# Kernel tuning notes

Measured on AMD Instinct MI355X. Metric: run time of the kernel, lower is better.

## Reference

```python
import jax, jax.numpy as jnp
import numpy as np

N_NODES = 100000
N_EDGES = 1600000
F_IN, HID, N_CLS = 128, 64, 40


def gcn_conv(x, src, dst, W, b, n_nodes):
    # x: [N, Fin] -> [N, Fout]; edges already include self-loops.
    h = x @ W  # [N, Fout]
    ones = jnp.ones_like(src, dtype=h.dtype)
    deg = jax.ops.segment_sum(ones, dst, num_segments=n_nodes)  # [N]
    dinv = jnp.where(deg > 0, jax.lax.rsqrt(deg), 0.0)
    norm = dinv[src] * dinv[dst]  # [E]
    msg = h[src] * norm[:, None]  # gather + scale
    out = jax.ops.segment_sum(msg, dst, num_segments=n_nodes)  # scatter-sum
    return out + b


def setup_inputs() -> dict:
    key = jax.random.key(0)
    ks = jax.random.split(key, 8)
    x = jax.random.normal(ks[0], (N_NODES, F_IN), dtype=jnp.float32)
    edge_index = jax.random.randint(ks[1], (2, N_EDGES), 0, N_NODES, dtype=jnp.int64)

    def glorot(k, fi, fo):
        s = float(np.sqrt(6.0 / (fi + fo)))
        return jax.random.uniform(k, (fi, fo), jnp.float32, -s, s)

    return {
        "x": x,
        "edge_index": edge_index,
        "W1": glorot(ks[2], F_IN, HID), "b1": jnp.zeros((HID,), jnp.float32),
        "W2": glorot(ks[3], HID, HID), "b2": jnp.zeros((HID,), jnp.float32),
        "W3": glorot(ks[4], HID, N_CLS), "b3": jnp.zeros((N_CLS,), jnp.float32),
    }


def reference(x, edge_index, W1, b1, W2, b2, W3, b3):
    n = x.shape[0]
    loop = jnp.arange(n, dtype=edge_index.dtype)
    src = jnp.concatenate([edge_index[0], loop])  # add self-loops
    dst = jnp.concatenate([edge_index[1], loop])
    # layer 1..3: GCNConv -> relu -> dropout(eval: identity)
    h = jax.nn.relu(gcn_conv(x, src, dst, W1, b1, n))
    h = jax.nn.relu(gcn_conv(h, src, dst, W2, b2, n))
    h = jax.nn.relu(gcn_conv(h, src, dst, W3, b3, n))
    return jax.nn.log_softmax(h, axis=1)
```

## Files before the change

kernel.cpp:

```cpp
#include <hip/hip_runtime.h>
#include <math.h>

typedef _Float16 half8   __attribute__((ext_vector_type(8)));
typedef float    float4v __attribute__((ext_vector_type(4)));

#define NPB   196
#define CAP   4096
#define DIVM  342393ull

static __device__ __forceinline__ unsigned short f32_to_f16u(float f) {
    _Float16 h = (_Float16)f;
    return __builtin_bit_cast(unsigned short, h);
}

static __device__ __forceinline__ int bkt_of(int d) {
    return (int)(((unsigned long long)(unsigned)d * DIVM) >> 26);
}


__global__ __launch_bounds__(256) void bin_edges(
    const int* __restrict__ src, const int* __restrict__ dst,
    int* __restrict__ bcur, unsigned int* __restrict__ bint, int E, int NB)
{
    __shared__ int h[512];
    __shared__ int rbase[512];
    const int tid = threadIdx.x;
    h[tid] = 0; h[tid + 256] = 0;
    __syncthreads();

    const int chunk = (E + (int)gridDim.x - 1) / (int)gridDim.x;
    const int base  = (int)blockIdx.x * chunk;
    int end = base + chunk; if (end > E) end = E;

    for (int i = base + tid; i < end; i += 256)
        atomicAdd(&h[bkt_of(dst[i])], 1);
    __syncthreads();

    for (int j = tid; j < NB; j += 256) {
        int c = h[j];
        rbase[j] = c ? atomicAdd(&bcur[j], c) : 0;
        h[j] = 0;
    }
    __syncthreads();

    for (int i = base + tid; i < end; i += 256) {
        int d = dst[i];
        int bkt = bkt_of(d);
        int low = d - bkt * NPB;
        int pos = rbase[bkt] + atomicAdd(&h[bkt], 1);
        if (pos < CAP)
            bint[(size_t)bkt * CAP + pos] =
                ((unsigned int)src[i] << 8) | (unsigned int)low;
    }
}


__global__ __launch_bounds__(256) void build_csr(
    const unsigned int* __restrict__ bint, const int* __restrict__ bcur,
    int2* __restrict__ rp2, float* __restrict__ dinv, int* __restrict__ es, int n)
{
    __shared__ int cnt[256];
    __shared__ int sc[256];
    __shared__ int cur[256];
    const int b = blockIdx.x, tid = threadIdx.x;
    int total = bcur[b]; if (total > CAP) total = CAP;
    const unsigned int* bp = bint + (size_t)b * CAP;
    int* ep = es + (size_t)b * CAP;
    const int base = b * CAP;

    cnt[tid] = 0;
    __syncthreads();
    for (int i = tid; i < total; i += 256)
        atomicAdd(&cnt[bp[i] & 255], 1);
    __syncthreads();

    int v = (tid < NPB) ? cnt[tid] : 0;
    sc[tid] = v;
    __syncthreads();
    for (int off = 1; off < 256; off <<= 1) {
        int x = (tid >= off) ? sc[tid - off] : 0;
        __syncthreads();
        sc[tid] += x;
        __syncthreads();
    }
    int excl = sc[tid] - v;
    int node = b * NPB + tid;
    if (tid < NPB && node < n) {
        rp2[node]  = make_int2(base + excl, base + excl + v);
        dinv[node] = rsqrtf((float)(v + 1));
    }
    cur[tid] = excl;
    __syncthreads();

    for (int i = tid; i < total; i += 256) {
        unsigned int p = bp[i];
        int pos = atomicAdd(&cur[p & 255], 1);
        ep[pos] = (int)(p >> 8);
    }
}


template<int KK, int NT, int STRIDE, int MOUT, bool INF32>
__global__ __launch_bounds__(256) void gemm_t(
    const void* __restrict__ Xin, const float* __restrict__ W,
    const float* __restrict__ dinv, unsigned short* __restrict__ H, int n)
{
    constexpr int KS = KK >> 5;
    __shared__ __align__(16) unsigned short ldsA[4 * KS * 512];
    const int tid = threadIdx.x;
    const int n0  = blockIdx.x * 64;
    const int wv   = tid >> 6;
    const int lane = tid & 63;
    const int q8 = (lane >> 4) << 3, mc = lane & 15;

    half8 bf[NT * KS];
    #pragma unroll
    for (int u = 0; u < NT; ++u)
        #pragma unroll
        for (int s = 0; s < KS; ++s) {
            const int col = (u << 4) + mc;
            #pragma unroll
            for (int j = 0; j < 8; ++j)
                bf[u * KS + s][j] = (col < MOUT)
                    ? (_Float16)W[((s << 5) + q8 + j) * MOUT + col] : (_Float16)0;
        }

    {
        const int rl = tid >> 3;
        const int kl = tid & 7;
        #pragma unroll
        for (int rb = 0; rb < 64; rb += 32) {
            int r = rl + rb;
            int node = n0 + r;
            int t = r >> 4, m = r & 15;
            if (INF32) {
                #pragma unroll
                for (int kq8 = 0; kq8 < (KK >> 2); kq8 += 8) {
                    int k0 = (kl + kq8) << 2;
                    unsigned short h[4] = {0, 0, 0, 0};
                    if (node < n) {
                        const float* xp = (const float*)Xin + (size_t)node * KK + k0;
                        float4v v = *(const float4v*)xp;
                        #pragma unroll
                        for (int i = 0; i < 4; ++i) h[i] = f32_to_f16u(v[i]);
                    }
                    int s = k0 >> 5, q = (k0 >> 3) & 3, j0 = k0 & 7;
                    int lds_lane = (q << 4) | m;
                    unsigned short* p = &ldsA[((t * KS + s) << 9) + (lds_lane << 3) + j0];
                    *(uint2*)p = make_uint2((unsigned)h[0] | ((unsigned)h[1] << 16),
                                            (unsigned)h[2] | ((unsigned)h[3] << 16));
                }
            } else {
                uint4 v = make_uint4(0, 0, 0, 0);
                if (node < n)
                    v = *(const uint4*)((const unsigned short*)Xin + (size_t)node * KK + (kl << 3));
                int k0 = kl << 3;
                int s = k0 >> 5, q = (k0 >> 3) & 3;
                unsigned short* p = &ldsA[((t * KS + s) << 9) + ((((q << 4) | m)) << 3)];
                *(uint4*)p = v;
            }
        }
    }

    __syncthreads();

    float4v acc[NT];
    #pragma unroll
    for (int u = 0; u < NT; ++u) acc[u] = (float4v){0.f, 0.f, 0.f, 0.f};

    #pragma unroll
    for (int s = 0; s < KS; ++s) {
        half8 a = *(const half8*)&ldsA[((wv * KS + s) << 9) + (lane << 3)];
        #pragma unroll
        for (int u = 0; u < NT; ++u)
            acc[u] = __builtin_amdgcn_mfma_f32_16x16x32_f16(a, bf[u * KS + s], acc[u], 0, 0, 0);
    }

    const int quad = lane >> 4;
    #pragma unroll
    for (int reg = 0; reg < 4; ++reg) {
        int node = n0 + (wv << 4) + (quad << 2) + reg;
        if (node >= n) continue;
        float dv = dinv[node];
        #pragma unroll
        for (int u = 0; u < NT; ++u) {
            int col = (u << 4) + mc;
            if (col < MOUT)
                H[(size_t)node * STRIDE + col] = f32_to_f16u(acc[u][reg] * dv);
        }
    }
}


template<int MOUT, int ROWU4>
__global__ __launch_bounds__(256) void gather_t(
    const int2* __restrict__ rp2, const int* __restrict__ es,
    const unsigned short* __restrict__ H, const float* __restrict__ dinv,
    const float* __restrict__ bias, unsigned short* __restrict__ Aout, int n)
{
    const int lane   = threadIdx.x & 63;
    const int half   = lane >> 5;
    const int lane32 = lane & 31;
    const int slot   = (lane >> 3) & 3;
    const int c8     = lane & 7;
    const bool act   = c8 < ROWU4;
    const uint4* H4  = (const uint4*)H;

    float bi[8];
    #pragma unroll
    for (int i = 0; i < 8; ++i) bi[i] = bias[(c8 << 3) + i];

    const half8 hz = {(_Float16)0, (_Float16)0, (_Float16)0, (_Float16)0,
                      (_Float16)0, (_Float16)0, (_Float16)0, (_Float16)0};

    const int TW2 = (int)(gridDim.x << 3);
    for (int nb = (((int)blockIdx.x << 2) + ((int)threadIdx.x >> 6)) << 1; nb < n; nb += TW2) {
        const int node = nb + half;
        const int2 e = rp2[node];
        const float dv = dinv[node];

        half8 hacc = hz;
        if (slot == 0 && act)
            hacc = __builtin_bit_cast(half8, H4[(size_t)node * ROWU4 + c8]);

        for (int cb = e.x; cb < e.y; cb += 32) {
            const int rem = e.y - cb;
            int eidx = cb + lane32; if (eidx > e.y - 1) eidx = e.y - 1;
            const int ei = es[eidx];
            #pragma unroll
            for (int j = 0; j < 8; ++j) {
                const int idx = (j << 2) + slot;
                const int s = __shfl(ei, (half << 5) + idx, 64);
                if (idx < rem && act)
                    hacc = hacc + __builtin_bit_cast(half8, H4[(size_t)s * ROWU4 + c8]);
            }
        }

        #pragma unroll
        for (int step = 8; step <= 16; step <<= 1) {
            uint4 u = __builtin_bit_cast(uint4, hacc);
            uint4 o;
            o.x = __shfl_xor(u.x, step, 64);
            o.y = __shfl_xor(u.y, step, 64);
            o.z = __shfl_xor(u.z, step, 64);
            o.w = __shfl_xor(u.w, step, 64);
            hacc = hacc + __builtin_bit_cast(half8, o);
        }

        if (slot == 0) {
            unsigned short o[8];
            #pragma unroll
            for (int i = 0; i < 8; ++i)
                o[i] = f32_to_f16u(fmaxf((float)hacc[i] * dv + bi[i], 0.0f));
            uint4 w;
            w.x = (unsigned int)o[0] | ((unsigned int)o[1] << 16);
            w.y = (unsigned int)o[2] | ((unsigned int)o[3] << 16);
            w.z = (unsigned int)o[4] | ((unsigned int)o[5] << 16);
            w.w = (unsigned int)o[6] | ((unsigned int)o[7] << 16);
            ((uint4*)Aout)[(size_t)node * 8 + c8] = w;
        }
    }
}


template<int MOUT, int ROWU4>
__global__ __launch_bounds__(256) void gather_softmax(
    const int2* __restrict__ rp2, const int* __restrict__ es,
    const unsigned short* __restrict__ H, const float* __restrict__ dinv,
    const float* __restrict__ bias, float* __restrict__ out, int n)
{
    const int lane   = threadIdx.x & 63;
    const int half   = lane >> 5;
    const int lane32 = lane & 31;
    const int slot   = (lane >> 3) & 3;
    const int c8     = lane & 7;
    const bool act   = c8 < ROWU4;
    const uint4* H4  = (const uint4*)H;

    float bi[8];
    #pragma unroll
    for (int i = 0; i < 8; ++i) {
        int col = (c8 << 3) + i;
        bi[i] = (col < MOUT) ? bias[col] : 0.0f;
    }

    const half8 hz = {(_Float16)0, (_Float16)0, (_Float16)0, (_Float16)0,
                      (_Float16)0, (_Float16)0, (_Float16)0, (_Float16)0};

    const int TW2 = (int)(gridDim.x << 3);
    for (int nb = (((int)blockIdx.x << 2) + ((int)threadIdx.x >> 6)) << 1; nb < n; nb += TW2) {
        const int node = nb + half;
        const int2 e = rp2[node];
        const float dv = dinv[node];

        half8 hacc = hz;
        if (slot == 0 && act)
            hacc = __builtin_bit_cast(half8, H4[(size_t)node * ROWU4 + c8]);

        for (int cb = e.x; cb < e.y; cb += 32) {
            const int rem = e.y - cb;
            int eidx = cb + lane32; if (eidx > e.y - 1) eidx = e.y - 1;
            const int ei = es[eidx];
            #pragma unroll
            for (int j = 0; j < 8; ++j) {
                const int idx = (j << 2) + slot;
                const int s = __shfl(ei, (half << 5) + idx, 64);
                if (idx < rem && act)
                    hacc = hacc + __builtin_bit_cast(half8, H4[(size_t)s * ROWU4 + c8]);
            }
        }

        #pragma unroll
        for (int step = 8; step <= 16; step <<= 1) {
            uint4 u = __builtin_bit_cast(uint4, hacc);
            uint4 o;
            o.x = __shfl_xor(u.x, step, 64);
            o.y = __shfl_xor(u.y, step, 64);
            o.z = __shfl_xor(u.z, step, 64);
            o.w = __shfl_xor(u.w, step, 64);
            hacc = hacc + __builtin_bit_cast(half8, o);
        }

        float z[8]; float m = -INFINITY;
        #pragma unroll
        for (int i = 0; i < 8; ++i) {
            int col = (c8 << 3) + i;
            z[i] = (col < MOUT && act) ? fmaxf((float)hacc[i] * dv + bi[i], 0.0f)
                                       : -INFINITY;
            m = fmaxf(m, z[i]);
        }
        m = fmaxf(m, __shfl_xor(m, 1, 64));
        m = fmaxf(m, __shfl_xor(m, 2, 64));
        m = fmaxf(m, __shfl_xor(m, 4, 64));
        float s = 0.0f;
        #pragma unroll
        for (int i = 0; i < 8; ++i) s += expf(z[i] - m);
        s += __shfl_xor(s, 1, 64);
        s += __shfl_xor(s, 2, 64);
        s += __shfl_xor(s, 4, 64);
        float ls = logf(s) + m;
        if (slot == 0 && c8 < (MOUT + 7) / 8) {
            float* op = out + (size_t)node * MOUT + (c8 << 3);
            float4v o0 = {z[0] - ls, z[1] - ls, z[2] - ls, z[3] - ls};
            float4v o1 = {z[4] - ls, z[5] - ls, z[6] - ls, z[7] - ls};
            *(float4v*)op = o0;
            *(float4v*)(op + 4) = o1;
        }
    }
}


extern "C" void kernel_launch(void* const* d_in, const int* in_sizes, int n_in,
                              void* d_out, int out_size, void* d_ws, size_t ws_size,
                              hipStream_t stream)
{
    const float* x  = (const float*)d_in[0];
    const int*   ei = (const int*)  d_in[1];
    const float* W1 = (const float*)d_in[2];
    const float* b1 = (const float*)d_in[3];
    const float* W2 = (const float*)d_in[4];
    const float* b2 = (const float*)d_in[5];
    const float* W3 = (const float*)d_in[6];
    const float* b3 = (const float*)d_in[7];

    const int F_IN = 128;
    const int n = in_sizes[0] / F_IN;
    const int E = in_sizes[1] / 2;
    const int* src = ei;
    const int* dst = ei + E;
    float* out = (float*)d_out;

    const int NB = (n + NPB - 1) / NPB;

    auto align = [](size_t v) { return (v + 255) & ~(size_t)255; };
    char* w = (char*)d_ws;
    size_t off = 0;
    float*          dinv = (float*)(w + off);          off = align(off + (size_t)n * 4);
    unsigned short* H1   = (unsigned short*)(w + off); off = align(off + (size_t)n * 64 * 2);
    unsigned short* A    = (unsigned short*)(w + off); off = align(off + (size_t)n * 64 * 2);
    unsigned short* H3   = (unsigned short*)(w + off); off = align(off + (size_t)n * 40 * 2);
    int2*           rp2  = (int2*)(w + off);           off = align(off + (size_t)n * 8);
    int*            es   = (int*)(w + off);            off = align(off + (size_t)NB * CAP * 4);
    unsigned int*   bint = (unsigned int*)(w + off);   off = align(off + (size_t)NB * CAP * 4);
    int*            bcur = (int*)(w + off);            off = align(off + (size_t)1024 * 4);
    unsigned short* H2   = H1;

    const int BLK = 256;
    auto cdiv = [](int a, int b) { return (a + b - 1) / b; };
    const int GB = cdiv(n, 64);
    const int GG = 2048;

    hipMemsetAsync(bcur, 0, (size_t)1024 * 4, stream);
    bin_edges<<<512, BLK, 0, stream>>>(src, dst, bcur, bint, E, NB);
    build_csr<<<NB, BLK, 0, stream>>>(bint, bcur, rp2, dinv, es, n);

    gemm_t<128, 4, 64, 64, true><<<GB, BLK, 0, stream>>>(x, W1, dinv, H1, n);
    gather_t<64, 8><<<GG, BLK, 0, stream>>>(rp2, es, H1, dinv, b1, A, n);

    gemm_t<64, 4, 64, 64, false><<<GB, BLK, 0, stream>>>(A, W2, dinv, H2, n);
    gather_t<64, 8><<<GG, BLK, 0, stream>>>(rp2, es, H2, dinv, b2, A, n);

    gemm_t<64, 3, 40, 40, false><<<GB, BLK, 0, stream>>>(A, W3, dinv, H3, n);
    gather_softmax<40, 5><<<GG, BLK, 0, stream>>>(rp2, es, H3, dinv, b3, out, n);
}
```

Baseline: 283.1 us.

## Stage edge binning and CSR build through LDS for coalesced global writes

Buckets change from 196 nodes per bucket (chosen with a magic-multiply divide) to 256 nodes per bucket using a shift. Each bin_edges block now takes a fixed 8192-edge chunk read with int4 loads. It sorts payloads locally in LDS by bucket using a prefix scan, then writes them out linearly so the global scatter lands in contiguous runs. build_csr likewise stages the bucket's edges in LDS and writes the sorted source list back contiguously. This is meant to cut the cost of uncoalesced scattered global writes, in exchange for more LDS per block (lower occupancy) and a larger bucket capacity.

```diff
diff --git a/kernel.cpp b/kernel.cpp
--- a/kernel.cpp
+++ b/kernel.cpp
@@ -4,53 +4,88 @@
 typedef _Float16 half8   __attribute__((ext_vector_type(8)));
 typedef float    float4v __attribute__((ext_vector_type(4)));
 
-#define NPB   196
-#define CAP   4096
-#define DIVM  342393ull
+#define CAP   6144
+#define EPB   8192
 
 static __device__ __forceinline__ unsigned short f32_to_f16u(float f) {
     _Float16 h = (_Float16)f;
     return __builtin_bit_cast(unsigned short, h);
 }
 
-static __device__ __forceinline__ int bkt_of(int d) {
-    return (int)(((unsigned long long)(unsigned)d * DIVM) >> 26);
-}
-
 
 __global__ __launch_bounds__(256) void bin_edges(
     const int* __restrict__ src, const int* __restrict__ dst,
     int* __restrict__ bcur, unsigned int* __restrict__ bint, int E, int NB)
 {
+    __shared__ unsigned int pay[EPB];
+    __shared__ unsigned int targ[EPB];
     __shared__ int h[512];
+    __shared__ int h2[512];
+    __shared__ int sc[512];
     __shared__ int rbase[512];
-    const int tid = threadIdx.x;
+
+    const int tid  = threadIdx.x;
+    const int base = (int)blockIdx.x * EPB;
+    int end = base + EPB; if (end > E) end = E;
+    const int total = end - base;
+    const int L4 = total & ~3;
+
     h[tid] = 0; h[tid + 256] = 0;
-    __syncthreads();
-
-    const int chunk = (E + (int)gridDim.x - 1) / (int)gridDim.x;
-    const int base  = (int)blockIdx.x * chunk;
-    int end = base + chunk; if (end > E) end = E;
-
-    for (int i = base + tid; i < end; i += 256)
-        atomicAdd(&h[bkt_of(dst[i])], 1);
-    __syncthreads();
+    h2[tid] = 0; h2[tid + 256] = 0;
+    __syncthreads();
+
+    for (int i = tid << 2; i < L4; i += 1024) {
+        int4 d4 = *(const int4*)(dst + base + i);
+        atomicAdd(&h[d4.x >> 8], 1);
+        atomicAdd(&h[d4.y >> 8], 1);
+        atomicAdd(&h[d4.z >> 8], 1);
+        atomicAdd(&h[d4.w >> 8], 1);
+    }
+    for (int i = L4 + tid; i < total; i += 256)
+        atomicAdd(&h[dst[base + i] >> 8], 1);
+    __syncthreads();
+
+    int v0 = h[tid], v1 = h[tid + 256];
+    sc[tid] = v0; sc[tid + 256] = v1;
+    __syncthreads();
+    for (int off = 1; off < 512; off <<= 1) {
+        int x0 = (tid >= off) ? sc[tid - off] : 0;
+        int x1 = (tid + 256 >= off) ? sc[tid + 256 - off] : 0;
+        __syncthreads();
+        sc[tid] += x0; sc[tid + 256] += x1;
+        __syncthreads();
+    }
 
     for (int j = tid; j < NB; j += 256) {
         int c = h[j];
         rbase[j] = c ? atomicAdd(&bcur[j], c) : 0;
-        h[j] = 0;
-    }
-    __syncthreads();
-
-    for (int i = base + tid; i < end; i += 256) {
-        int d = dst[i];
-        int bkt = bkt_of(d);
-        int low = d - bkt * NPB;
-        int pos = rbase[bkt] + atomicAdd(&h[bkt], 1);
-        if (pos < CAP)
-            bint[(size_t)bkt * CAP + pos] =
-                ((unsigned int)src[i] << 8) | (unsigned int)low;
+    }
+    __syncthreads();
+
+    {
+        auto place = [&](int d, int s) {
+            int bkt  = d >> 8;
+            int rank = atomicAdd(&h2[bkt], 1);
+            int loc  = sc[bkt] - h[bkt] + rank;
+            pay[loc] = ((unsigned int)s << 8) | (unsigned int)(d & 255);
+            unsigned int t = (unsigned int)(rbase[bkt] + rank);
+            targ[loc] = (t < (unsigned int)CAP)
+                      ? (unsigned int)bkt * CAP + t : 0xFFFFFFFFu;
+        };
+        for (int i = tid << 2; i < L4; i += 1024) {
+            int4 d4 = *(const int4*)(dst + base + i);
+            int4 s4 = *(const int4*)(src + base + i);
+            place(d4.x, s4.x); place(d4.y, s4.y);
+            place(d4.z, s4.z); place(d4.w, s4.w);
+        }
+        for (int i = L4 + tid; i < total; i += 256)
+            place(dst[base + i], src[base + i]);
+    }
+    __syncthreads();
+
+    for (int i = tid; i < total; i += 256) {
+        unsigned int t = targ[i];
+        if (t != 0xFFFFFFFFu) bint[t] = pay[i];
     }
 }
 
@@ -62,6 +97,8 @@
     __shared__ int cnt[256];
     __shared__ int sc[256];
     __shared__ int cur[256];
+    __shared__ unsigned int pin[CAP];
+    __shared__ int pout[CAP];
     const int b = blockIdx.x, tid = threadIdx.x;
     int total = bcur[b]; if (total > CAP) total = CAP;
     const unsigned int* bp = bint + (size_t)b * CAP;
@@ -70,11 +107,14 @@
 
     cnt[tid] = 0;
     __syncthreads();
-    for (int i = tid; i < total; i += 256)
-        atomicAdd(&cnt[bp[i] & 255], 1);
-    __syncthreads();
-
-    int v = (tid < NPB) ? cnt[tid] : 0;
+    for (int i = tid; i < total; i += 256) {
+        unsigned int v = bp[i];
+        pin[i] = v;
+        atomicAdd(&cnt[v & 255], 1);
+    }
+    __syncthreads();
+
+    int v = cnt[tid];
     sc[tid] = v;
     __syncthreads();
     for (int off = 1; off < 256; off <<= 1) {
@@ -84,8 +124,8 @@
         __syncthreads();
     }
     int excl = sc[tid] - v;
-    int node = b * NPB + tid;
-    if (tid < NPB && node < n) {
+    int node = (b << 8) + tid;
+    if (node < n) {
         rp2[node]  = make_int2(base + excl, base + excl + v);
         dinv[node] = rsqrtf((float)(v + 1));
     }
@@ -93,10 +133,14 @@
     __syncthreads();
 
     for (int i = tid; i < total; i += 256) {
-        unsigned int p = bp[i];
-        int pos = atomicAdd(&cur[p & 255], 1);
-        ep[pos] = (int)(p >> 8);
-    }
+        unsigned int p = pin[i];
+        int r = atomicAdd(&cur[p & 255], 1);
+        pout[r] = (int)(p >> 8);
+    }
+    __syncthreads();
+
+    for (int i = tid; i < total; i += 256)
+        ep[i] = pout[i];
 }
 
 
@@ -370,7 +414,7 @@
     const int* dst = ei + E;
     float* out = (float*)d_out;
 
-    const int NB = (n + NPB - 1) / NPB;
+    const int NB = (n + 255) >> 8;
 
     auto align = [](size_t v) { return (v + 255) & ~(size_t)255; };
     char* w = (char*)d_ws;
@@ -382,16 +426,17 @@
     int2*           rp2  = (int2*)(w + off);           off = align(off + (size_t)n * 8);
     int*            es   = (int*)(w + off);            off = align(off + (size_t)NB * CAP * 4);
     unsigned int*   bint = (unsigned int*)(w + off);   off = align(off + (size_t)NB * CAP * 4);
-    int*            bcur = (int*)(w + off);            off = align(off + (size_t)1024 * 4);
+    int*            bcur = (int*)(w + off);            off = align(off + (size_t)512 * 4);
     unsigned short* H2   = H1;
 
     const int BLK = 256;
     auto cdiv = [](int a, int b) { return (a + b - 1) / b; };
+    const int EB = cdiv(E, EPB);
     const int GB = cdiv(n, 64);
     const int GG = 2048;
 
-    hipMemsetAsync(bcur, 0, (size_t)1024 * 4, stream);
-    bin_edges<<<512, BLK, 0, stream>>>(src, dst, bcur, bint, E, NB);
+    hipMemsetAsync(bcur, 0, (size_t)512 * 4, stream);
+    bin_edges<<<EB, BLK, 0, stream>>>(src, dst, bcur, bint, E, NB);
     build_csr<<<NB, BLK, 0, stream>>>(bint, bcur, rp2, dinv, es, n);
 
     gemm_t<128, 4, 64, 64, true><<<GB, BLK, 0, stream>>>(x, W1, dinv, H1, n);
```

New measurement: 270.5 us. 4.5% less time.
